# Optimization experiments

Hardware: AMD Instinct MI355X
Metric: run time of the kernel (lower is better)

The kernel has to match this reference:

```python
import jax, jax.numpy as jnp
import numpy as np

B, S, IN, OUT = 16, 512, 1024, 4096
QMAX = 127.0

def setup_inputs() -> dict:
    key = jax.random.key(0)
    k1, k2, k3, k4 = jax.random.split(key, 4)
    x = jax.random.normal(k1, (B, S, IN), dtype=jnp.float32)
    # int8 weights stored as int32 spec but clamped to int8 range, cast to int8
    weight_int8 = jax.random.randint(k2, (OUT, IN), -128, 128, dtype=jnp.int32).astype(jnp.int8)
    weight_scale = jax.random.uniform(k3, (OUT,), dtype=jnp.float32, minval=1e-4, maxval=0.02)
    bias = jax.random.normal(k4, (OUT,), dtype=jnp.float32)
    return {"x": x, "weight_int8": weight_int8, "weight_scale": weight_scale, "bias": bias}

def reference(x, weight_int8, weight_scale, bias):
    # dynamic per-token abs-max quantization
    abs_max = jnp.max(jnp.abs(x), axis=-1, keepdims=True)          # [B,S,1]
    input_scale = abs_max / QMAX
    input_scale = jnp.where(input_scale == 0, 1.0, input_scale)
    x_int8 = jnp.clip(jnp.round(x / input_scale), -128.0, 127.0)   # float-emulated int8
    # int8 matmul emulated in float (as in the original F.linear on .float())
    out_i32 = jnp.einsum('bsi,oi->bso', x_int8, weight_int8.astype(jnp.float32))
    out = out_i32 * weight_scale * input_scale                     # dequantize
    out = out + bias
    return out
```

## Files before the change

kernel.cpp:

```cpp
#include <hip/hip_runtime.h>


#define M_TOT 8192
#define N_TOT 4096
#define K_TOT 1024
#define QMAXF 127.0f

#define BM 256
#define BN 256
#define BK 128
#define NKT (K_TOT / BK)

typedef int i32x4 __attribute__((ext_vector_type(4)));

__global__ __launch_bounds__(256) void prep(const float* __restrict__ x,
                                            const int* __restrict__ w32,
                                            signed char* __restrict__ xq,
                                            signed char* __restrict__ w8,
                                            float* __restrict__ iscale) {
  const int b = blockIdx.x;
  const int t = threadIdx.x;

  if (b < M_TOT) {
    const float4 v = reinterpret_cast<const float4*>(x)[(size_t)b * 256 + t];
    float m = fmaxf(fmaxf(fabsf(v.x), fabsf(v.y)), fmaxf(fabsf(v.z), fabsf(v.w)));
#pragma unroll
    for (int off = 32; off >= 1; off >>= 1) m = fmaxf(m, __shfl_xor(m, off, 64));

    __shared__ float wmax[4];
    const int lane = t & 63, wid = t >> 6;
    if (lane == 0) wmax[wid] = m;
    __syncthreads();
    const float amax = fmaxf(fmaxf(wmax[0], wmax[1]), fmaxf(wmax[2], wmax[3]));

    float scale = amax / QMAXF;
    if (scale == 0.0f) scale = 1.0f;

    int qi;
    signed char* qb = reinterpret_cast<signed char*>(&qi);
    qb[0] = (signed char)(int)fminf(fmaxf(rintf(v.x / scale), -128.0f), 127.0f);
    qb[1] = (signed char)(int)fminf(fmaxf(rintf(v.y / scale), -128.0f), 127.0f);
    qb[2] = (signed char)(int)fminf(fmaxf(rintf(v.z / scale), -128.0f), 127.0f);
    qb[3] = (signed char)(int)fminf(fmaxf(rintf(v.w / scale), -128.0f), 127.0f);
    reinterpret_cast<int*>(xq)[(size_t)b * 256 + t] = qi;

    if (t == 0) iscale[b] = scale;
  } else {
    const int i = (b - M_TOT) * 256 + t;
    const int4 v = reinterpret_cast<const int4*>(w32)[i];
    const int packed = (v.x & 0xFF) | ((v.y & 0xFF) << 8) |
                       ((v.z & 0xFF) << 16) | (v.w << 24);
    reinterpret_cast<int*>(w8)[i] = packed;
  }
}

__device__ __forceinline__ void gload_lds16(const void* g, void* l) {
  __builtin_amdgcn_global_load_lds(
      (const __attribute__((address_space(1))) unsigned int*)g,
      (__attribute__((address_space(3))) unsigned int*)l, 16, 0, 0);
}

__global__ __launch_bounds__(512, 2) void int8_gemm(const signed char* __restrict__ xq,
                                                    const signed char* __restrict__ w,
                                                    const float* __restrict__ iscale,
                                                    const float* __restrict__ wscale,
                                                    const float* __restrict__ bias,
                                                    float* __restrict__ out) {
  __shared__ __attribute__((aligned(16))) signed char As[2][BM][BK];
  __shared__ __attribute__((aligned(16))) signed char Bs[2][BN][BK];

  const int t = threadIdx.x;
  const int lane = t & 63;
  const int wid = t >> 6;
  const int wm = wid >> 2;
  const int wn = wid & 3;

  const int bid = blockIdx.x;
  const int swz = (bid & 7) * 64 + (bid >> 3);
  const int m0 = (swz >> 4) * BM;
  const int n0 = (swz & 15) * BN;

  const int srow = t >> 3;
  const int scol_swz = ((t & 7) * 16) ^ ((srow & 7) << 4);

  auto stage = [&](int buf, int kt) {
    const int k0 = kt * BK;
#pragma unroll
    for (int c = 0; c < 4; ++c) {
      gload_lds16(xq + (size_t)(m0 + c * 64 + srow) * K_TOT + k0 + scol_swz,
                  &As[buf][c * 64][0] + t * 16);
      gload_lds16(w + (size_t)(n0 + c * 64 + srow) * K_TOT + k0 + scol_swz,
                  &Bs[buf][c * 64][0] + t * 16);
    }
  };

  i32x4 acc[8][4] = {};

  stage(0, 0);
  __syncthreads();

  for (int kt = 0; kt < NKT; ++kt) {
    const int cur = kt & 1;
    if (kt + 1 < NKT) stage(cur ^ 1, kt + 1);

#pragma unroll
    for (int ks = 0; ks < 2; ++ks) {
      const int kofs = ks * 64 + ((lane >> 4) * 16);
      i32x4 a[8], b[4];
#pragma unroll
      for (int f = 0; f < 8; ++f) {
        const int r = wm * 128 + f * 16 + (lane & 15);
        a[f] = *reinterpret_cast<const i32x4*>(&As[cur][r][kofs ^ ((r & 7) << 4)]);
      }
#pragma unroll
      for (int g = 0; g < 4; ++g) {
        const int r = wn * 64 + g * 16 + (lane & 15);
        b[g] = *reinterpret_cast<const i32x4*>(&Bs[cur][r][kofs ^ ((r & 7) << 4)]);
      }
#pragma unroll
      for (int f = 0; f < 8; ++f)
#pragma unroll
        for (int g = 0; g < 4; ++g)
          acc[f][g] = __builtin_amdgcn_mfma_i32_16x16x64_i8(a[f], b[g], acc[f][g], 0, 0, 0);
    }
    __syncthreads();
  }

  const int col = lane & 15;
  const int rq = lane >> 4;
  float wsc[4], bv[4];
#pragma unroll
  for (int g = 0; g < 4; ++g) {
    const int gn = n0 + wn * 64 + g * 16 + col;
    wsc[g] = wscale[gn];
    bv[g] = bias[gn];
  }
#pragma unroll
  for (int f = 0; f < 8; ++f) {
    const int gmb = m0 + wm * 128 + f * 16 + rq * 4;
#pragma unroll
    for (int i = 0; i < 4; ++i) {
      const int gm = gmb + i;
      const float isc = iscale[gm];
      float* rowp = out + (size_t)gm * N_TOT + n0 + wn * 64 + col;
#pragma unroll
      for (int g = 0; g < 4; ++g)
        rowp[g * 16] = (float)acc[f][g][i] * wsc[g] * isc + bv[g];
    }
  }
}

extern "C" void kernel_launch(void* const* d_in, const int* in_sizes, int n_in,
                              void* d_out, int out_size, void* d_ws, size_t ws_size,
                              hipStream_t stream) {
  const float* x = (const float*)d_in[0];
  const int* w32 = (const int*)d_in[1];
  const float* wscale = (const float*)d_in[2];
  const float* bias = (const float*)d_in[3];
  float* out = (float*)d_out;

  signed char* xq = (signed char*)d_ws;
  float* iscale = (float*)((char*)d_ws + (size_t)M_TOT * K_TOT);
  signed char* w8 = (signed char*)((char*)d_ws + (size_t)M_TOT * K_TOT + M_TOT * 4);

  const int pack_blocks = (N_TOT * K_TOT / 4) / 256;
  prep<<<M_TOT + pack_blocks, 256, 0, stream>>>(x, w32, xq, w8, iscale);
  int8_gemm<<<dim3((M_TOT / BM) * (N_TOT / BN)), 512, 0, stream>>>(xq, w8, iscale, wscale, bias, out);
}
```

Measured before the change: 63.93 us.

## Split A/B staging and interleave loads with MFMA phases using fine-grained barriers

Restructures the GEMM main loop so that A and B tiles are staged separately and at different points of each iteration. B for the next tile is issued after a partial vmcnt wait, and A for tile+2 is written into the just-consumed buffer mid-iteration, with explicit s_barrier calls between phases. MFMA blocks are wrapped in s_setprio to favour compute waves. The aim is to overlap global-to-LDS loads with matrix math and to replace full __syncthreads with lighter waits, at the risk of subtle buffer-reuse races if the vmcnt counts or barrier placement are wrong.

```diff
diff --git a/kernel.cpp b/kernel.cpp
--- a/kernel.cpp
+++ b/kernel.cpp
@@ -83,47 +83,108 @@
   const int srow = t >> 3;
   const int scol_swz = ((t & 7) * 16) ^ ((srow & 7) << 4);
 
-  auto stage = [&](int buf, int kt) {
+  auto stageA = [&](int buf, int kt) {
     const int k0 = kt * BK;
 #pragma unroll
-    for (int c = 0; c < 4; ++c) {
+    for (int c = 0; c < 4; ++c)
       gload_lds16(xq + (size_t)(m0 + c * 64 + srow) * K_TOT + k0 + scol_swz,
                   &As[buf][c * 64][0] + t * 16);
+  };
+  auto stageB = [&](int buf, int kt) {
+    const int k0 = kt * BK;
+#pragma unroll
+    for (int c = 0; c < 4; ++c)
       gload_lds16(w + (size_t)(n0 + c * 64 + srow) * K_TOT + k0 + scol_swz,
                   &Bs[buf][c * 64][0] + t * 16);
-    }
   };
 
+  const int kql = (lane >> 4) * 16;
+
   i32x4 acc[8][4] = {};
 
-  stage(0, 0);
-  __syncthreads();
-
-  for (int kt = 0; kt < NKT; ++kt) {
-    const int cur = kt & 1;
-    if (kt + 1 < NKT) stage(cur ^ 1, kt + 1);
-
+  stageA(0, 0);
+  stageB(0, 0);
+  stageA(1, 1);
+
+  for (int U = 0; U < NKT - 1; ++U) {
+    const int cur = U & 1;
+
+    asm volatile("s_waitcnt vmcnt(4)\n\ts_barrier" ::: "memory");
+    stageB(cur ^ 1, U + 1);
+
+    i32x4 a0[8], b0[4];
+#pragma unroll
+    for (int f = 0; f < 8; ++f) {
+      const int r = wm * 128 + f * 16 + (lane & 15);
+      a0[f] = *reinterpret_cast<const i32x4*>(&As[cur][r][kql ^ ((r & 7) << 4)]);
+    }
+#pragma unroll
+    for (int g = 0; g < 4; ++g) {
+      const int r = wn * 64 + g * 16 + (lane & 15);
+      b0[g] = *reinterpret_cast<const i32x4*>(&Bs[cur][r][kql ^ ((r & 7) << 4)]);
+    }
+    __builtin_amdgcn_s_setprio(1);
+#pragma unroll
+    for (int f = 0; f < 8; ++f)
+#pragma unroll
+      for (int g = 0; g < 4; ++g)
+        acc[f][g] = __builtin_amdgcn_mfma_i32_16x16x64_i8(a0[f], b0[g], acc[f][g], 0, 0, 0);
+    __builtin_amdgcn_s_setprio(0);
+
+    asm volatile("s_barrier" ::: "memory");
+    i32x4 a1[8], b1[4];
+#pragma unroll
+    for (int f = 0; f < 8; ++f) {
+      const int r = wm * 128 + f * 16 + (lane & 15);
+      a1[f] = *reinterpret_cast<const i32x4*>(&As[cur][r][(64 + kql) ^ ((r & 7) << 4)]);
+    }
+#pragma unroll
+    for (int g = 0; g < 4; ++g) {
+      const int r = wn * 64 + g * 16 + (lane & 15);
+      b1[g] = *reinterpret_cast<const i32x4*>(&Bs[cur][r][(64 + kql) ^ ((r & 7) << 4)]);
+    }
+    __builtin_amdgcn_s_setprio(1);
+#pragma unroll
+    for (int f = 0; f < 8; ++f)
+#pragma unroll
+      for (int g = 0; g < 2; ++g)
+        acc[f][g] = __builtin_amdgcn_mfma_i32_16x16x64_i8(a1[f], b1[g], acc[f][g], 0, 0, 0);
+    __builtin_amdgcn_s_setprio(0);
+
+    asm volatile("s_barrier" ::: "memory");
+    if (U + 2 < NKT) stageA(cur, U + 2);
+    __builtin_amdgcn_s_setprio(1);
+#pragma unroll
+    for (int f = 0; f < 8; ++f)
+#pragma unroll
+      for (int g = 2; g < 4; ++g)
+        acc[f][g] = __builtin_amdgcn_mfma_i32_16x16x64_i8(a1[f], b1[g], acc[f][g], 0, 0, 0);
+    __builtin_amdgcn_s_setprio(0);
+  }
+
+  {
+    const int cur = (NKT - 1) & 1;
+    asm volatile("s_waitcnt vmcnt(0)\n\ts_barrier" ::: "memory");
+    i32x4 a0[8], b0[4];
 #pragma unroll
     for (int ks = 0; ks < 2; ++ks) {
-      const int kofs = ks * 64 + ((lane >> 4) * 16);
-      i32x4 a[8], b[4];
+      const int kofs = ks * 64 + kql;
 #pragma unroll
       for (int f = 0; f < 8; ++f) {
         const int r = wm * 128 + f * 16 + (lane & 15);
-        a[f] = *reinterpret_cast<const i32x4*>(&As[cur][r][kofs ^ ((r & 7) << 4)]);
+        a0[f] = *reinterpret_cast<const i32x4*>(&As[cur][r][kofs ^ ((r & 7) << 4)]);
       }
 #pragma unroll
       for (int g = 0; g < 4; ++g) {
         const int r = wn * 64 + g * 16 + (lane & 15);
-        b[g] = *reinterpret_cast<const i32x4*>(&Bs[cur][r][kofs ^ ((r & 7) << 4)]);
+        b0[g] = *reinterpret_cast<const i32x4*>(&Bs[cur][r][kofs ^ ((r & 7) << 4)]);
       }
 #pragma unroll
       for (int f = 0; f < 8; ++f)
 #pragma unroll
         for (int g = 0; g < 4; ++g)
-          acc[f][g] = __builtin_amdgcn_mfma_i32_16x16x64_i8(a[f], b[g], acc[f][g], 0, 0, 0);
-    }
-    __syncthreads();
+          acc[f][g] = __builtin_amdgcn_mfma_i32_16x16x64_i8(a0[f], b0[g], acc[f][g], 0, 0, 0);
+    }
   }
 
   const int col = lane & 15;
```

New measurement: 63.51 us. Within noise of the previous version (-0.7%).

## Restructure int8 GEMM main loop into quarter-tile staged pipeline with priority MFMA

Applied to the files above, without the earlier changes.

Replaces the simple double-buffered k-loop with a fully unrolled schedule. Each k-tile is split into four MFMA quadrants, and the next tile's global-to-LDS loads are issued in halves between them. Explicit vmcnt/lgkmcnt waits, barriers, sched_barrier and setprio are meant to overlap LDS reads and global loads with MFMA work. It also interleaves the warp-to-row/column mapping, changes block-to-XCD tile assignment for L2 locality, and uses nontemporal output stores. The hand-placed waits and barriers are fragile: a wrong vmcnt count could read stale LDS data, and the extra barriers add synchronisation points.

```diff
diff --git a/kernel.cpp b/kernel.cpp
--- a/kernel.cpp
+++ b/kernel.cpp
@@ -59,6 +59,59 @@
       (const __attribute__((address_space(1))) unsigned int*)g,
       (__attribute__((address_space(3))) unsigned int*)l, 16, 0, 0);
 }
+
+#define MFMA16(h, nh)                                                        \
+  __builtin_amdgcn_s_setprio(1);                                             \
+  _Pragma("unroll") for (int j = 0; j < 4; ++j)                              \
+  _Pragma("unroll") for (int jb = 0; jb < 2; ++jb)                           \
+  _Pragma("unroll") for (int ks = 0; ks < 2; ++ks)                           \
+      acc[(h) * 4 + j][(nh) * 2 + jb] = __builtin_amdgcn_mfma_i32_16x16x64_i8( \
+          a[j * 2 + ks], bb[(nh)][jb * 2 + ks], acc[(h) * 4 + j][(nh) * 2 + jb], \
+          0, 0, 0);                                                          \
+  __builtin_amdgcn_s_setprio(0);
+
+#define TILE(U, DO_STAGE, VM0, VM1)                                          \
+  {                                                                          \
+    const int c = (U) & 1;                                                   \
+                             \
+    asm volatile("s_waitcnt vmcnt(" VM0 ")" ::: "memory");                   \
+    __builtin_amdgcn_s_barrier();                                            \
+    _Pragma("unroll") for (int j = 0; j < 4; ++j) {                          \
+      a[j * 2] = rdA(c, j, 0);                                               \
+      a[j * 2 + 1] = rdA(c, j, 1);                                           \
+    }                                                                        \
+    _Pragma("unroll") for (int jb = 0; jb < 2; ++jb) {                       \
+      bb[0][jb * 2] = rdB(c, jb, 0);                                         \
+      bb[0][jb * 2 + 1] = rdB(c, jb, 1);                                     \
+    }                                                                        \
+    if (DO_STAGE) { stA(c ^ 1, (U) + 1, 0); stB(c ^ 1, (U) + 1, 0); }        \
+    asm volatile("s_waitcnt lgkmcnt(0)" ::: "memory");                       \
+    __builtin_amdgcn_sched_barrier(0);                                       \
+    MFMA16(0, 0)                                                             \
+                                      \
+    asm volatile("s_waitcnt vmcnt(" VM1 ")" ::: "memory");                   \
+    __builtin_amdgcn_s_barrier();                                            \
+    _Pragma("unroll") for (int jb = 0; jb < 2; ++jb) {                       \
+      bb[1][jb * 2] = rdB(c, 2 + jb, 0);                                     \
+      bb[1][jb * 2 + 1] = rdB(c, 2 + jb, 1);                                 \
+    }                                                                        \
+    if (DO_STAGE) { stA(c ^ 1, (U) + 1, 1); stB(c ^ 1, (U) + 1, 1); }        \
+    asm volatile("s_waitcnt lgkmcnt(0)" ::: "memory");                       \
+    __builtin_amdgcn_sched_barrier(0);                                       \
+    MFMA16(0, 1)                                                             \
+                                      \
+    __builtin_amdgcn_s_barrier();                                            \
+    _Pragma("unroll") for (int j = 0; j < 4; ++j) {                          \
+      a[j * 2] = rdA(c, 4 + j, 0);                                           \
+      a[j * 2 + 1] = rdA(c, 4 + j, 1);                                       \
+    }                                                                        \
+    asm volatile("s_waitcnt lgkmcnt(0)" ::: "memory");                       \
+    __builtin_amdgcn_sched_barrier(0);                                       \
+    MFMA16(1, 0)                                                             \
+                      \
+    __builtin_amdgcn_s_barrier();                                            \
+    MFMA16(1, 1)                                                             \
+  }
 
 __global__ __launch_bounds__(512, 2) void int8_gemm(const signed char* __restrict__ xq,
                                                     const signed char* __restrict__ w,
@@ -76,76 +129,78 @@
   const int wn = wid & 3;
 
   const int bid = blockIdx.x;
-  const int swz = (bid & 7) * 64 + (bid >> 3);
-  const int m0 = (swz >> 4) * BM;
-  const int n0 = (swz & 15) * BN;
+  const int xcd = bid & 7, li = bid >> 3;
+  const int mt = (xcd >> 1) * 8 + (li >> 3);
+  const int nt = (xcd & 1) * 8 + (li & 7);
+  const int m0 = mt * BM, n0 = nt * BN;
 
   const int srow = t >> 3;
   const int scol_swz = ((t & 7) * 16) ^ ((srow & 7) << 4);
 
-  auto stage = [&](int buf, int kt) {
+  auto stA = [&](int buf, int kt, int h) {
     const int k0 = kt * BK;
 #pragma unroll
-    for (int c = 0; c < 4; ++c) {
-      gload_lds16(xq + (size_t)(m0 + c * 64 + srow) * K_TOT + k0 + scol_swz,
-                  &As[buf][c * 64][0] + t * 16);
-      gload_lds16(w + (size_t)(n0 + c * 64 + srow) * K_TOT + k0 + scol_swz,
-                  &Bs[buf][c * 64][0] + t * 16);
+    for (int cc = 0; cc < 2; ++cc) {
+      const int row = h * 128 + cc * 64 + srow;
+      gload_lds16(xq + (size_t)(m0 + row) * K_TOT + k0 + scol_swz,
+                  &As[buf][h * 128 + cc * 64][0] + t * 16);
     }
   };
+  auto stB = [&](int buf, int kt, int h) {
+    const int k0 = kt * BK;
+#pragma unroll
+    for (int cc = 0; cc < 2; ++cc) {
+      const int row = h * 128 + cc * 64 + srow;
+      gload_lds16(w + (size_t)(n0 + row) * K_TOT + k0 + scol_swz,
+                  &Bs[buf][h * 128 + cc * 64][0] + t * 16);
+    }
+  };
+
+  const int lr = lane & 15;
+  const int kq = (lane >> 4) * 16;
+  const int sx = (lane & 7) << 4;
+  auto rdA = [&](int buf, int f, int ks) -> i32x4 {
+    const int r = f * 32 + wm * 16 + lr;
+    return *reinterpret_cast<const i32x4*>(&As[buf][r][(ks * 64 + kq) ^ sx]);
+  };
+  auto rdB = [&](int buf, int g, int ks) -> i32x4 {
+    const int r = g * 64 + wn * 16 + lr;
+    return *reinterpret_cast<const i32x4*>(&Bs[buf][r][(ks * 64 + kq) ^ sx]);
+  };
 
   i32x4 acc[8][4] = {};
-
-  stage(0, 0);
-  __syncthreads();
-
-  for (int kt = 0; kt < NKT; ++kt) {
-    const int cur = kt & 1;
-    if (kt + 1 < NKT) stage(cur ^ 1, kt + 1);
-
-#pragma unroll
-    for (int ks = 0; ks < 2; ++ks) {
-      const int kofs = ks * 64 + ((lane >> 4) * 16);
-      i32x4 a[8], b[4];
-#pragma unroll
-      for (int f = 0; f < 8; ++f) {
-        const int r = wm * 128 + f * 16 + (lane & 15);
-        a[f] = *reinterpret_cast<const i32x4*>(&As[cur][r][kofs ^ ((r & 7) << 4)]);
-      }
-#pragma unroll
-      for (int g = 0; g < 4; ++g) {
-        const int r = wn * 64 + g * 16 + (lane & 15);
-        b[g] = *reinterpret_cast<const i32x4*>(&Bs[cur][r][kofs ^ ((r & 7) << 4)]);
-      }
-#pragma unroll
-      for (int f = 0; f < 8; ++f)
-#pragma unroll
-        for (int g = 0; g < 4; ++g)
-          acc[f][g] = __builtin_amdgcn_mfma_i32_16x16x64_i8(a[f], b[g], acc[f][g], 0, 0, 0);
-    }
-    __syncthreads();
-  }
+  i32x4 a[8], bb[2][4];
+
+  stA(0, 0, 0); stB(0, 0, 0);
+  stA(0, 0, 1); stB(0, 0, 1);
+
+#pragma unroll
+  for (int U = 0; U < NKT - 1; ++U) {
+    TILE(U, 1, "4", "4")
+  }
+  TILE(NKT - 1, 0, "4", "0")
 
   const int col = lane & 15;
   const int rq = lane >> 4;
   float wsc[4], bv[4];
 #pragma unroll
   for (int g = 0; g < 4; ++g) {
-    const int gn = n0 + wn * 64 + g * 16 + col;
+    const int gn = n0 + g * 64 + wn * 16 + col;
     wsc[g] = wscale[gn];
     bv[g] = bias[gn];
   }
 #pragma unroll
   for (int f = 0; f < 8; ++f) {
-    const int gmb = m0 + wm * 128 + f * 16 + rq * 4;
+    const int gmb = m0 + f * 32 + wm * 16 + rq * 4;
 #pragma unroll
     for (int i = 0; i < 4; ++i) {
       const int gm = gmb + i;
       const float isc = iscale[gm];
-      float* rowp = out + (size_t)gm * N_TOT + n0 + wn * 64 + col;
+      float* rowp = out + (size_t)gm * N_TOT + n0 + wn * 16 + col;
 #pragma unroll
       for (int g = 0; g < 4; ++g)
-        rowp[g * 16] = (float)acc[f][g][i] * wsc[g] * isc + bv[g];
+        __builtin_nontemporal_store((float)acc[f][g][i] * wsc[g] * isc + bv[g],
+                                    rowp + g * 64);
     }
   }
 }
```

Result: slower. 82.13 us (+28.5%).

## Restructure int8 GEMM main loop into fine-grained interleaved load/MFMA pipeline

Applied to the files above, without the earlier changes.

Halves BK to 64 and splits each K-tile into four MFMA quarter-phases. Each phase issues one slice of the next tile's global-to-LDS loads, guarded by explicit vmcnt waits and raw s_barrier, with s_setprio raised around the MFMA bursts. The goal is to overlap memory traffic with matrix work more evenly and lower register pressure. It also changes the warp-to-fragment mapping and LDS swizzle, remaps blocks to XCDs for L2 locality, and uses nontemporal output stores. The hand-tuned waitcnt values and barrier placement carry a correctness risk if the load-count accounting is off.

```diff
diff --git a/kernel.cpp b/kernel.cpp
--- a/kernel.cpp
+++ b/kernel.cpp
@@ -8,7 +8,7 @@
 
 #define BM 256
 #define BN 256
-#define BK 128
+#define BK 64
 #define NKT (K_TOT / BK)
 
 typedef int i32x4 __attribute__((ext_vector_type(4)));
@@ -60,6 +60,41 @@
       (__attribute__((address_space(3))) unsigned int*)l, 16, 0, 0);
 }
 
+#define MFMA8(h, nh)                                                          \
+  __builtin_amdgcn_s_setprio(1);                                              \
+  _Pragma("unroll") for (int j = 0; j < 4; ++j)                               \
+  _Pragma("unroll") for (int jb = 0; jb < 2; ++jb)                            \
+      acc[(h) * 4 + j][(nh) * 2 + jb] = __builtin_amdgcn_mfma_i32_16x16x64_i8( \
+          a[j], bb[(nh) * 2 + jb], acc[(h) * 4 + j][(nh) * 2 + jb], 0, 0, 0); \
+  __builtin_amdgcn_s_setprio(0);
+
+#define TILE(U, DO_STAGE, VM0, VM1, VM2)                                      \
+  {                                                                           \
+    const int c = (U) & 1;                                                    \
+                                 \
+    asm volatile("s_waitcnt vmcnt(" VM0 ")" ::: "memory");                    \
+    __builtin_amdgcn_s_barrier();                                             \
+    _Pragma("unroll") for (int j = 0; j < 4; ++j) a[j] = rdA(c, j);           \
+    bb[0] = rdB(c, 0); bb[1] = rdB(c, 1);                                     \
+    if (DO_STAGE) stA(c ^ 1, (U) + 1, 0);                                     \
+    MFMA8(0, 0)                                                               \
+                                     \
+    asm volatile("s_waitcnt vmcnt(" VM1 ")" ::: "memory");                    \
+    __builtin_amdgcn_s_barrier();                                             \
+    bb[2] = rdB(c, 2); bb[3] = rdB(c, 3);                                     \
+    if (DO_STAGE) stB(c ^ 1, (U) + 1, 0);                                     \
+    MFMA8(0, 1)                                                               \
+                                     \
+    asm volatile("s_waitcnt vmcnt(" VM2 ")" ::: "memory");                    \
+    __builtin_amdgcn_s_barrier();                                             \
+    _Pragma("unroll") for (int j = 0; j < 4; ++j) a[j] = rdA(c, 4 + j);       \
+    if (DO_STAGE) stB(c ^ 1, (U) + 1, 1);                                     \
+    MFMA8(1, 0)                                                               \
+                         \
+    if (DO_STAGE) stA(c ^ 1, (U) + 1, 1);                                     \
+    MFMA8(1, 1)                                                               \
+  }
+
 __global__ __launch_bounds__(512, 2) void int8_gemm(const signed char* __restrict__ xq,
                                                     const signed char* __restrict__ w,
                                                     const float* __restrict__ iscale,
@@ -76,76 +111,66 @@
   const int wn = wid & 3;
 
   const int bid = blockIdx.x;
-  const int swz = (bid & 7) * 64 + (bid >> 3);
-  const int m0 = (swz >> 4) * BM;
-  const int n0 = (swz & 15) * BN;
+  const int xcd = bid & 7, li = bid >> 3;
+  const int mt = (xcd >> 1) * 8 + (li >> 3);
+  const int nt = (xcd & 1) * 8 + (li & 7);
+  const int m0 = mt * BM, n0 = nt * BN;
 
-  const int srow = t >> 3;
-  const int scol_swz = ((t & 7) * 16) ^ ((srow & 7) << 4);
+  const int srow = t >> 2;
+  const int scol_swz = ((t & 3) * 16) ^ (((srow >> 1) & 3) << 4);
 
-  auto stage = [&](int buf, int kt) {
-    const int k0 = kt * BK;
-#pragma unroll
-    for (int c = 0; c < 4; ++c) {
-      gload_lds16(xq + (size_t)(m0 + c * 64 + srow) * K_TOT + k0 + scol_swz,
-                  &As[buf][c * 64][0] + t * 16);
-      gload_lds16(w + (size_t)(n0 + c * 64 + srow) * K_TOT + k0 + scol_swz,
-                  &Bs[buf][c * 64][0] + t * 16);
-    }
+  auto stA = [&](int buf, int kt, int h) {
+    gload_lds16(xq + (size_t)(m0 + h * 128 + srow) * K_TOT + kt * BK + scol_swz,
+                &As[buf][h * 128][0] + t * 16);
+  };
+  auto stB = [&](int buf, int kt, int h) {
+    gload_lds16(w + (size_t)(n0 + h * 128 + srow) * K_TOT + kt * BK + scol_swz,
+                &Bs[buf][h * 128][0] + t * 16);
+  };
+
+  const int lr = lane & 15;
+  const int rcol = (((lane >> 4) * 16)) ^ (((lr >> 1) & 3) << 4);
+  auto rdA = [&](int buf, int f) -> i32x4 {
+    return *reinterpret_cast<const i32x4*>(&As[buf][f * 32 + wm * 16 + lr][rcol]);
+  };
+  auto rdB = [&](int buf, int g) -> i32x4 {
+    return *reinterpret_cast<const i32x4*>(&Bs[buf][g * 64 + wn * 16 + lr][rcol]);
   };
 
   i32x4 acc[8][4] = {};
+  i32x4 a[4], bb[4];
 
-  stage(0, 0);
-  __syncthreads();
+  stA(0, 0, 0);
+  stB(0, 0, 0);
+  stB(0, 0, 1);
+  stA(0, 0, 1);
 
-  for (int kt = 0; kt < NKT; ++kt) {
-    const int cur = kt & 1;
-    if (kt + 1 < NKT) stage(cur ^ 1, kt + 1);
-
-#pragma unroll
-    for (int ks = 0; ks < 2; ++ks) {
-      const int kofs = ks * 64 + ((lane >> 4) * 16);
-      i32x4 a[8], b[4];
-#pragma unroll
-      for (int f = 0; f < 8; ++f) {
-        const int r = wm * 128 + f * 16 + (lane & 15);
-        a[f] = *reinterpret_cast<const i32x4*>(&As[cur][r][kofs ^ ((r & 7) << 4)]);
-      }
-#pragma unroll
-      for (int g = 0; g < 4; ++g) {
-        const int r = wn * 64 + g * 16 + (lane & 15);
-        b[g] = *reinterpret_cast<const i32x4*>(&Bs[cur][r][kofs ^ ((r & 7) << 4)]);
-      }
-#pragma unroll
-      for (int f = 0; f < 8; ++f)
-#pragma unroll
-        for (int g = 0; g < 4; ++g)
-          acc[f][g] = __builtin_amdgcn_mfma_i32_16x16x64_i8(a[f], b[g], acc[f][g], 0, 0, 0);
-    }
-    __syncthreads();
+  for (int U = 0; U < NKT - 1; ++U) {
+    TILE(U, 1, "2", "2", "2")
   }
+  TILE(NKT - 1, 0, "2", "1", "0")
 
   const int col = lane & 15;
   const int rq = lane >> 4;
   float wsc[4], bv[4];
 #pragma unroll
   for (int g = 0; g < 4; ++g) {
-    const int gn = n0 + wn * 64 + g * 16 + col;
+    const int gn = n0 + g * 64 + wn * 16 + col;
     wsc[g] = wscale[gn];
     bv[g] = bias[gn];
   }
 #pragma unroll
   for (int f = 0; f < 8; ++f) {
-    const int gmb = m0 + wm * 128 + f * 16 + rq * 4;
+    const int gmb = m0 + f * 32 + wm * 16 + rq * 4;
 #pragma unroll
     for (int i = 0; i < 4; ++i) {
       const int gm = gmb + i;
       const float isc = iscale[gm];
-      float* rowp = out + (size_t)gm * N_TOT + n0 + wn * 64 + col;
+      float* rowp = out + (size_t)gm * N_TOT + n0 + wn * 16 + col;
 #pragma unroll
       for (int g = 0; g < 4; ++g)
-        rowp[g * 16] = (float)acc[f][g][i] * wsc[g] * isc + bv[g];
+        __builtin_nontemporal_store((float)acc[f][g][i] * wsc[g] * isc + bv[g],
+                                    rowp + g * 64);
     }
   }
 }
```

Measured after the change: 84.55 us. 32.3% more time.
